# Optimization experiments

Measured on AMD Instinct MI355X. Metric: run time of the kernel, lower is better.

Reference implementation:

```python
import jax, jax.numpy as jnp
import numpy as np

GRID_SIDES = (16, 32, 64)  # levels=3, base_grid_size=16, expansion=2.0, grid_dimensions=2
BATCH, INPUT_DIM = 8192, 256


def setup_inputs() -> dict:
    key = jax.random.key(0)
    k0, k1, k2, k3 = jax.random.split(key, 4)
    x = jax.random.normal(k0, (BATCH, INPUT_DIM), dtype=jnp.float32)
    w1 = jax.random.normal(k1, (GRID_SIDES[0] ** 2, INPUT_DIM), dtype=jnp.float32)
    w2 = jax.random.normal(k2, (GRID_SIDES[1] ** 2, INPUT_DIM), dtype=jnp.float32)
    w3 = jax.random.normal(k3, (GRID_SIDES[2] ** 2, INPUT_DIM), dtype=jnp.float32)
    return {"x": x, "w1": w1, "w2": w2, "w3": w3}


def _som_level(x, w, side):
    # Squared Euclidean distances (B, N) via the expanded form; N = side*side.
    d2 = (
        jnp.sum(x * x, axis=1, keepdims=True)
        - 2.0 * (x @ w.T)
        + jnp.sum(w * w, axis=1)
    )
    bmu_flat = jnp.argmin(d2, axis=1)  # (B,)
    coords = jnp.stack(jnp.unravel_index(bmu_flat, (side, side)), axis=-1)  # (B, 2)
    # Quantization error = exact Euclidean distance to the BMU prototype.
    diff = x - w[bmu_flat]  # (B, D)
    q_err = jnp.sqrt(jnp.sum(diff * diff, axis=1))  # (B,)
    return coords, q_err


def reference(x, w1, w2, w3):
    c1, q1 = _som_level(x, w1, GRID_SIDES[0])
    c2, q2 = _som_level(x, w2, GRID_SIDES[1])
    c3, q3 = _som_level(x, w3, GRID_SIDES[2])
    return (c1, c2, c3, q1, q2, q3)
```

## Files before the change

kernel.cpp:

```cpp
#include <hip/hip_runtime.h>
#include <hip/hip_fp16.h>
#include <stdint.h>

#define DIM 256
#define KE  768
#define NW  5376

typedef _Float16 half8 __attribute__((ext_vector_type(8)));
typedef float floatx4 __attribute__((ext_vector_type(4)));

#define WS_WE_OFF    12582912
#define WS_WNORM_OFF 20840448
#define WS_XNORM_OFF 20861952
#define WS_BEST_OFF  20894720

__global__ __launch_bounds__(256) void conv_kernel(
    const float* __restrict__ x, const float* __restrict__ w1,
    const float* __restrict__ w2, const float* __restrict__ w3,
    ushort* __restrict__ Xe, ushort* __restrict__ We,
    float* __restrict__ wnorm, float* __restrict__ xnorm) {
  int task = blockIdx.x * 4 + (threadIdx.x >> 6);
  int lane = threadIdx.x & 63;
  const float* src; ushort* dst; float* ndst; int isx;
  if (task < 8192) {
    src = x + (size_t)task * DIM; dst = Xe + (size_t)task * KE;
    ndst = xnorm + task; isx = 1;
  } else {
    int wi = task - 8192;
    if (wi < 256)       src = w1 + (size_t)wi * DIM;
    else if (wi < 1280) src = w2 + (size_t)(wi - 256) * DIM;
    else                src = w3 + (size_t)(wi - 1280) * DIM;
    dst = We + (size_t)wi * KE; ndst = wnorm + wi; isx = 0;
  }
  float4 v = *(const float4*)(src + lane * 4);
  float fv[4] = {v.x, v.y, v.z, v.w};
  float s = fv[0]*fv[0] + fv[1]*fv[1] + fv[2]*fv[2] + fv[3]*fv[3];
  #pragma unroll
  for (int o = 32; o > 0; o >>= 1) s += __shfl_xor(s, o);
  if (lane == 0) *ndst = s;

  ushort h[4], l[4];
  #pragma unroll
  for (int e = 0; e < 4; ++e) {
    __half hh = __float2half(fv[e]);
    float hf = __half2float(hh);
    __half ll = __float2half((fv[e] - hf) * 2048.0f);
    h[e] = __half_as_ushort(hh);
    l[e] = __half_as_ushort(ll);
  }
  ushort4 h4 = make_ushort4(h[0], h[1], h[2], h[3]);
  ushort4 l4 = make_ushort4(l[0], l[1], l[2], l[3]);
  if (isx) {
    *(ushort4*)(dst + lane * 4)        = h4;
    *(ushort4*)(dst + 256 + lane * 4)  = h4;
    *(ushort4*)(dst + 512 + lane * 4)  = l4;
  } else {
    *(ushort4*)(dst + lane * 4)        = h4;
    *(ushort4*)(dst + 256 + lane * 4)  = l4;
    *(ushort4*)(dst + 512 + lane * 4)  = h4;
  }
}

__global__ __launch_bounds__(256) void gemm_kernel(
    const ushort* __restrict__ Xe, const ushort* __restrict__ We,
    const float* __restrict__ xnorm, const float* __restrict__ wnorm,
    unsigned long long* __restrict__ best) {
  __shared__ __align__(16) ushort As[128 * 64];
  __shared__ __align__(16) ushort Bs[128 * 64];
  __shared__ unsigned long long red[2][128];

  const int cb = blockIdx.x;
  const int r0 = blockIdx.y * 128;
  const int n0 = cb * 128;
  int level, lbase;
  if (cb < 2)       { level = 0; lbase = 0; }
  else if (cb < 10) { level = 1; lbase = 256; }
  else              { level = 2; lbase = 1280; }

  const int t = threadIdx.x;
  const int w = t >> 6;
  const int lane = t & 63;
  const int ln = lane & 15, q = lane >> 4;
  const int wm = (w >> 1) * 64, wn = (w & 1) * 64;

  floatx4 acc[4][4];
  #pragma unroll
  for (int i = 0; i < 4; ++i)
    #pragma unroll
    for (int j = 0; j < 4; ++j) acc[i][j] = (floatx4)0.0f;

  for (int k0 = 0; k0 < KE; k0 += 64) {
    if (k0 == 256) {
      #pragma unroll
      for (int i = 0; i < 4; ++i)
        #pragma unroll
        for (int j = 0; j < 4; ++j) acc[i][j] *= 2048.0f;
    }
    #pragma unroll
    for (int it = 0; it < 4; ++it) {
      int p = it * 256 + t;
      int m = p >> 3;
      int c = (p & 7) ^ (m & 7);
      const ushort* ga = Xe + (size_t)(r0 + m) * KE + k0 + c * 8;
      const ushort* gb = We + (size_t)(n0 + m) * KE + k0 + c * 8;
      int lbase_chunks = it * 256 + (t & 192);
      __builtin_amdgcn_global_load_lds(
          (const __attribute__((address_space(1))) void*)ga,
          (__attribute__((address_space(3))) void*)(As + lbase_chunks * 8), 16, 0, 0);
      __builtin_amdgcn_global_load_lds(
          (const __attribute__((address_space(1))) void*)gb,
          (__attribute__((address_space(3))) void*)(Bs + lbase_chunks * 8), 16, 0, 0);
    }
    __syncthreads();
    #pragma unroll
    for (int s = 0; s < 2; ++s) {
      half8 a[4], b[4];
      #pragma unroll
      for (int mt = 0; mt < 4; ++mt) {
        int m = wm + mt * 16 + ln;
        int pos = m * 8 + ((s * 4 + q) ^ (m & 7));
        a[mt] = *(const half8*)&As[pos * 8];
      }
      #pragma unroll
      for (int nt = 0; nt < 4; ++nt) {
        int n = wn + nt * 16 + ln;
        int pos = n * 8 + ((s * 4 + q) ^ (n & 7));
        b[nt] = *(const half8*)&Bs[pos * 8];
      }
      #pragma unroll
      for (int mt = 0; mt < 4; ++mt)
        #pragma unroll
        for (int nt = 0; nt < 4; ++nt)
          acc[mt][nt] = __builtin_amdgcn_mfma_f32_16x16x32_f16(
              a[mt], b[nt], acc[mt][nt], 0, 0, 0);
    }
    __syncthreads();
  }

  float wnv[4];
  #pragma unroll
  for (int nt = 0; nt < 4; ++nt) wnv[nt] = wnorm[n0 + wn + nt * 16 + ln];

  #pragma unroll
  for (int mt = 0; mt < 4; ++mt) {
    #pragma unroll
    for (int r = 0; r < 4; ++r) {
      int rowl = wm + mt * 16 + q * 4 + r;
      float xnv = xnorm[r0 + rowl];
      unsigned long long bp = ~0ull;
      #pragma unroll
      for (int nt = 0; nt < 4; ++nt) {
        float d2 = fmaxf(xnv + wnv[nt] - acc[mt][nt][r] * 0.0009765625f, 0.0f);
        unsigned col = (unsigned)(n0 + wn + nt * 16 + ln - lbase);
        unsigned long long p =
            ((unsigned long long)__float_as_uint(d2) << 32) | col;
        bp = (p < bp) ? p : bp;
      }
      #pragma unroll
      for (int off = 1; off < 16; off <<= 1) {
        unsigned long long o = __shfl_xor(bp, off);
        bp = (o < bp) ? o : bp;
      }
      if (ln == 0) red[w & 1][rowl] = bp;
    }
  }
  __syncthreads();
  if (t < 128) {
    unsigned long long a = red[0][t], b = red[1][t];
    unsigned long long m = (a < b) ? a : b;
    atomicMin(&best[level * 8192 + r0 + t], m);
  }
}

__global__ __launch_bounds__(256) void finalize_kernel(
    const float* __restrict__ x, const float* __restrict__ w1,
    const float* __restrict__ w2, const float* __restrict__ w3,
    const unsigned long long* __restrict__ best, float* __restrict__ out) {
  int task = blockIdx.x * 4 + (threadIdx.x >> 6);
  int lane = threadIdx.x & 63;
  int level = task >> 13;
  int row = task & 8191;
  const float* w; unsigned side;
  if (level == 0)      { w = w1; side = 16; }
  else if (level == 1) { w = w2; side = 32; }
  else                 { w = w3; side = 64; }
  unsigned idx = (unsigned)(best[level * 8192 + row] & 0xFFFFFFFFull);
  float4 xv = *(const float4*)(x + (size_t)row * DIM + lane * 4);
  float4 wv = *(const float4*)(w + (size_t)idx * DIM + lane * 4);
  float dx = xv.x - wv.x, dy = xv.y - wv.y, dz = xv.z - wv.z, dw = xv.w - wv.w;
  float s = dx * dx + dy * dy + dz * dz + dw * dw;
  #pragma unroll
  for (int o = 32; o > 0; o >>= 1) s += __shfl_xor(s, o);
  if (lane == 0) {
    out[level * 16384 + row * 2 + 0] = (float)(idx / side);
    out[level * 16384 + row * 2 + 1] = (float)(idx % side);
    out[49152 + level * 8192 + row] = sqrtf(s);
  }
}

extern "C" void kernel_launch(void* const* d_in, const int* in_sizes, int n_in,
                              void* d_out, int out_size, void* d_ws, size_t ws_size,
                              hipStream_t stream) {
  const float* x  = (const float*)d_in[0];
  const float* w1 = (const float*)d_in[1];
  const float* w2 = (const float*)d_in[2];
  const float* w3 = (const float*)d_in[3];
  ushort* Xe = (ushort*)d_ws;
  ushort* We = (ushort*)((char*)d_ws + WS_WE_OFF);
  float* wnorm = (float*)((char*)d_ws + WS_WNORM_OFF);
  float* xnorm = (float*)((char*)d_ws + WS_XNORM_OFF);
  unsigned long long* best = (unsigned long long*)((char*)d_ws + WS_BEST_OFF);

  hipMemsetAsync(best, 0xFF, 24576 * sizeof(unsigned long long), stream);
  conv_kernel<<<3392, 256, 0, stream>>>(x, w1, w2, w3, Xe, We, wnorm, xnorm);
  gemm_kernel<<<dim3(42, 64), 256, 0, stream>>>(Xe, We, xnorm, wnorm, best);
  finalize_kernel<<<6144, 256, 0, stream>>>(x, w1, w2, w3, best, (float*)d_out);
}
```

Baseline: 175.0 us.

## Rewrite split-fp16 GEMM as 256x256 tile with multi-stage LDS pipeline

The distance GEMM now uses 512-thread blocks, each computing a 256x256 output tile. Operands are streamed through a four-slot LDS ring in 32-wide K chunks, with async global-to-LDS loads issued two chunks ahead, phase barriers and MFMA priority raising. The conversion kernel pre-scales the leading hi*hi segment (x by 64, w by 32) so the accumulator no longer needs the mid-loop multiply by 2048. The aim is more reuse per block and load latency hidden behind MFMA work, at the cost of larger LDS and register footprints and fragile hand-written wait counts.

```diff
diff --git a/kernel.cpp b/kernel.cpp
--- a/kernel.cpp
+++ b/kernel.cpp
@@ -39,119 +39,168 @@
   for (int o = 32; o > 0; o >>= 1) s += __shfl_xor(s, o);
   if (lane == 0) *ndst = s;
 
-  ushort h[4], l[4];
+  float scale = isx ? 64.0f : 32.0f;
+  ushort h[4], hs[4], l[4];
   #pragma unroll
   for (int e = 0; e < 4; ++e) {
     __half hh = __float2half(fv[e]);
     float hf = __half2float(hh);
-    __half ll = __float2half((fv[e] - hf) * 2048.0f);
-    h[e] = __half_as_ushort(hh);
-    l[e] = __half_as_ushort(ll);
+    h[e]  = __half_as_ushort(hh);
+    hs[e] = __half_as_ushort(__float2half(hf * scale));
+    l[e]  = __half_as_ushort(__float2half((fv[e] - hf) * 2048.0f));
   }
   ushort4 h4 = make_ushort4(h[0], h[1], h[2], h[3]);
+  ushort4 s4 = make_ushort4(hs[0], hs[1], hs[2], hs[3]);
   ushort4 l4 = make_ushort4(l[0], l[1], l[2], l[3]);
   if (isx) {
-    *(ushort4*)(dst + lane * 4)        = h4;
+    *(ushort4*)(dst + lane * 4)        = s4;
     *(ushort4*)(dst + 256 + lane * 4)  = h4;
     *(ushort4*)(dst + 512 + lane * 4)  = l4;
   } else {
-    *(ushort4*)(dst + lane * 4)        = h4;
+    *(ushort4*)(dst + lane * 4)        = s4;
     *(ushort4*)(dst + 256 + lane * 4)  = l4;
     *(ushort4*)(dst + 512 + lane * 4)  = h4;
   }
 }
 
-__global__ __launch_bounds__(256) void gemm_kernel(
+__global__ __launch_bounds__(512, 2) void gemm_kernel(
     const ushort* __restrict__ Xe, const ushort* __restrict__ We,
     const float* __restrict__ xnorm, const float* __restrict__ wnorm,
     unsigned long long* __restrict__ best) {
-  __shared__ __align__(16) ushort As[128 * 64];
-  __shared__ __align__(16) ushort Bs[128 * 64];
-  __shared__ unsigned long long red[2][128];
-
-  const int cb = blockIdx.x;
-  const int r0 = blockIdx.y * 128;
-  const int n0 = cb * 128;
-  int level, lbase;
-  if (cb < 2)       { level = 0; lbase = 0; }
-  else if (cb < 10) { level = 1; lbase = 256; }
-  else              { level = 2; lbase = 1280; }
+  __shared__ __align__(16) ushort AB[65536];
+  __shared__ unsigned long long red[4][256];
 
   const int t = threadIdx.x;
   const int w = t >> 6;
   const int lane = t & 63;
   const int ln = lane & 15, q = lane >> 4;
-  const int wm = (w >> 1) * 64, wn = (w & 1) * 64;
-
-  floatx4 acc[4][4];
-  #pragma unroll
-  for (int i = 0; i < 4; ++i)
+  const int wr = w >> 2, wc = w & 3;
+  const int r0 = blockIdx.x * 256;
+  const int cb = blockIdx.y;
+  const int n0 = cb << 8;
+  int level, lbase;
+  if (cb < 1)      { level = 0; lbase = 0; }
+  else if (cb < 5) { level = 1; lbase = 256; }
+  else             { level = 2; lbase = 1280; }
+
+  int aoff[2][4], boff[4];
+  #pragma unroll
+  for (int mh = 0; mh < 2; ++mh)
+    #pragma unroll
+    for (int mt = 0; mt < 4; ++mt) {
+      int ra = wr * 128 + mh * 64 + mt * 16 + ln;
+      aoff[mh][mt] = ra * 64 + ((q ^ ((ra >> 1) & 3)) << 4);
+    }
+  #pragma unroll
+  for (int nt = 0; nt < 4; ++nt) {
+    int rb = wc * 64 + nt * 16 + ln;
+    boff[nt] = 65536 + rb * 64 + ((q ^ ((rb >> 1) & 3)) << 4);
+  }
+  const char* ABb = (const char*)AB;
+
+  const int sr = (w << 4) + (lane >> 2);
+  const int sc = lane & 3;
+  const int sg = sc ^ ((sr >> 1) & 3);
+  const ushort* srcA0 = Xe + (size_t)(r0 + sr) * KE + sg * 8;
+  const ushort* srcB0 = We + (size_t)(n0 + sr) * KE + sg * 8;
+  const int ldsO0 = w << 9;
+  const int ldsO1 = 4096 + (w << 9);
+
+#define STAGE_A(hs_) do { const int sl_ = ((hs_) & 3) << 13; \
+    __builtin_amdgcn_global_load_lds( \
+        (const __attribute__((address_space(1))) void*)(srcA0 + (hs_) * 32), \
+        (__attribute__((address_space(3))) void*)(AB + sl_ + ldsO0), 16, 0, 0); \
+    __builtin_amdgcn_global_load_lds( \
+        (const __attribute__((address_space(1))) void*)(srcA0 + 128 * KE + (hs_) * 32), \
+        (__attribute__((address_space(3))) void*)(AB + sl_ + ldsO1), 16, 0, 0); \
+  } while (0)
+#define STAGE_B(hs_) do { const int sl_ = 32768 + (((hs_) & 3) << 13); \
+    __builtin_amdgcn_global_load_lds( \
+        (const __attribute__((address_space(1))) void*)(srcB0 + (hs_) * 32), \
+        (__attribute__((address_space(3))) void*)(AB + sl_ + ldsO0), 16, 0, 0); \
+    __builtin_amdgcn_global_load_lds( \
+        (const __attribute__((address_space(1))) void*)(srcB0 + 128 * KE + (hs_) * 32), \
+        (__attribute__((address_space(3))) void*)(AB + sl_ + ldsO1), 16, 0, 0); \
+  } while (0)
+
+  floatx4 acc[8][4];
+  #pragma unroll
+  for (int i = 0; i < 8; ++i)
     #pragma unroll
     for (int j = 0; j < 4; ++j) acc[i][j] = (floatx4)0.0f;
 
-  for (int k0 = 0; k0 < KE; k0 += 64) {
-    if (k0 == 256) {
-      #pragma unroll
-      for (int i = 0; i < 4; ++i)
-        #pragma unroll
-        for (int j = 0; j < 4; ++j) acc[i][j] *= 2048.0f;
-    }
-    #pragma unroll
-    for (int it = 0; it < 4; ++it) {
-      int p = it * 256 + t;
-      int m = p >> 3;
-      int c = (p & 7) ^ (m & 7);
-      const ushort* ga = Xe + (size_t)(r0 + m) * KE + k0 + c * 8;
-      const ushort* gb = We + (size_t)(n0 + m) * KE + k0 + c * 8;
-      int lbase_chunks = it * 256 + (t & 192);
-      __builtin_amdgcn_global_load_lds(
-          (const __attribute__((address_space(1))) void*)ga,
-          (__attribute__((address_space(3))) void*)(As + lbase_chunks * 8), 16, 0, 0);
-      __builtin_amdgcn_global_load_lds(
-          (const __attribute__((address_space(1))) void*)gb,
-          (__attribute__((address_space(3))) void*)(Bs + lbase_chunks * 8), 16, 0, 0);
-    }
-    __syncthreads();
-    #pragma unroll
-    for (int s = 0; s < 2; ++s) {
-      half8 a[4], b[4];
-      #pragma unroll
-      for (int mt = 0; mt < 4; ++mt) {
-        int m = wm + mt * 16 + ln;
-        int pos = m * 8 + ((s * 4 + q) ^ (m & 7));
-        a[mt] = *(const half8*)&As[pos * 8];
-      }
-      #pragma unroll
-      for (int nt = 0; nt < 4; ++nt) {
-        int n = wn + nt * 16 + ln;
-        int pos = n * 8 + ((s * 4 + q) ^ (n & 7));
-        b[nt] = *(const half8*)&Bs[pos * 8];
-      }
-      #pragma unroll
-      for (int mt = 0; mt < 4; ++mt)
-        #pragma unroll
-        for (int nt = 0; nt < 4; ++nt)
-          acc[mt][nt] = __builtin_amdgcn_mfma_f32_16x16x32_f16(
-              a[mt], b[nt], acc[mt][nt], 0, 0, 0);
-    }
-    __syncthreads();
-  }
+  half8 av[4], bv[4];
+
+  STAGE_A(0); STAGE_B(0); STAGE_A(1); STAGE_B(1);
+  asm volatile("s_waitcnt vmcnt(4)" ::: "memory");
+  __builtin_amdgcn_s_barrier();
+  __builtin_amdgcn_sched_barrier(0);
+
+#define PH0(h_, STG_) { \
+    const int sb_ = ((h_) & 3) << 14; \
+    _Pragma("unroll") for (int mt = 0; mt < 4; ++mt) \
+      av[mt] = *(const half8*)(ABb + sb_ + aoff[0][mt]); \
+    _Pragma("unroll") for (int nt = 0; nt < 4; ++nt) \
+      bv[nt] = *(const half8*)(ABb + sb_ + boff[nt]); \
+    if (STG_) STAGE_A((h_) + 2); \
+    __builtin_amdgcn_sched_barrier(0); \
+    __builtin_amdgcn_s_barrier(); \
+    __builtin_amdgcn_sched_barrier(0); \
+    __builtin_amdgcn_s_setprio(1); \
+    _Pragma("unroll") for (int mt = 0; mt < 4; ++mt) \
+      _Pragma("unroll") for (int nt = 0; nt < 4; ++nt) \
+        acc[mt][nt] = __builtin_amdgcn_mfma_f32_16x16x32_f16( \
+            av[mt], bv[nt], acc[mt][nt], 0, 0, 0); \
+    __builtin_amdgcn_s_setprio(0); \
+    __builtin_amdgcn_sched_barrier(0); \
+    __builtin_amdgcn_s_barrier(); \
+    __builtin_amdgcn_sched_barrier(0); \
+  }
+#define PH1(h_, STG_, VMS_) { \
+    const int sb_ = ((h_) & 3) << 14; \
+    _Pragma("unroll") for (int mt = 0; mt < 4; ++mt) \
+      av[mt] = *(const half8*)(ABb + sb_ + aoff[1][mt]); \
+    if (STG_) STAGE_B((h_) + 2); \
+    __builtin_amdgcn_sched_barrier(0); \
+    __builtin_amdgcn_s_barrier(); \
+    __builtin_amdgcn_sched_barrier(0); \
+    __builtin_amdgcn_s_setprio(1); \
+    _Pragma("unroll") for (int mt = 0; mt < 4; ++mt) \
+      _Pragma("unroll") for (int nt = 0; nt < 4; ++nt) \
+        acc[4 + mt][nt] = __builtin_amdgcn_mfma_f32_16x16x32_f16( \
+            av[mt], bv[nt], acc[4 + mt][nt], 0, 0, 0); \
+    __builtin_amdgcn_s_setprio(0); \
+    VMS_; \
+    __builtin_amdgcn_sched_barrier(0); \
+    __builtin_amdgcn_s_barrier(); \
+    __builtin_amdgcn_sched_barrier(0); \
+  }
+
+  #pragma unroll 1
+  for (int h = 0; h < 22; ++h) {
+    PH0(h, 1);
+    PH1(h, 1, asm volatile("s_waitcnt vmcnt(4)" ::: "memory"));
+  }
+  PH0(22, 0);
+  PH1(22, 0, asm volatile("s_waitcnt vmcnt(0)" ::: "memory"));
+  PH0(23, 0);
+  PH1(23, 0, );
 
   float wnv[4];
   #pragma unroll
-  for (int nt = 0; nt < 4; ++nt) wnv[nt] = wnorm[n0 + wn + nt * 16 + ln];
-
-  #pragma unroll
-  for (int mt = 0; mt < 4; ++mt) {
+  for (int nt = 0; nt < 4; ++nt) wnv[nt] = wnorm[n0 + wc * 64 + nt * 16 + ln];
+
+  #pragma unroll
+  for (int mtg = 0; mtg < 8; ++mtg) {
     #pragma unroll
     for (int r = 0; r < 4; ++r) {
-      int rowl = wm + mt * 16 + q * 4 + r;
+      int rowl = wr * 128 + mtg * 16 + q * 4 + r;
       float xnv = xnorm[r0 + rowl];
       unsigned long long bp = ~0ull;
       #pragma unroll
       for (int nt = 0; nt < 4; ++nt) {
-        float d2 = fmaxf(xnv + wnv[nt] - acc[mt][nt][r] * 0.0009765625f, 0.0f);
-        unsigned col = (unsigned)(n0 + wn + nt * 16 + ln - lbase);
+        float d2 = fmaxf(xnv + wnv[nt] - acc[mtg][nt][r] * 0.0009765625f, 0.0f);
+        unsigned col = (unsigned)(n0 + wc * 64 + nt * 16 + ln - lbase);
         unsigned long long p =
             ((unsigned long long)__float_as_uint(d2) << 32) | col;
         bp = (p < bp) ? p : bp;
@@ -161,13 +210,16 @@
         unsigned long long o = __shfl_xor(bp, off);
         bp = (o < bp) ? o : bp;
       }
-      if (ln == 0) red[w & 1][rowl] = bp;
+      if (ln == 0) red[wc][rowl] = bp;
     }
   }
   __syncthreads();
-  if (t < 128) {
-    unsigned long long a = red[0][t], b = red[1][t];
-    unsigned long long m = (a < b) ? a : b;
+  if (t < 256) {
+    unsigned long long m0 = red[0][t], m1 = red[1][t];
+    unsigned long long m2 = red[2][t], m3 = red[3][t];
+    unsigned long long m = m0 < m1 ? m0 : m1;
+    if (m2 < m) m = m2;
+    if (m3 < m) m = m3;
     atomicMin(&best[level * 8192 + r0 + t], m);
   }
 }
@@ -213,6 +265,6 @@
 
   hipMemsetAsync(best, 0xFF, 24576 * sizeof(unsigned long long), stream);
   conv_kernel<<<3392, 256, 0, stream>>>(x, w1, w2, w3, Xe, We, wnorm, xnorm);
-  gemm_kernel<<<dim3(42, 64), 256, 0, stream>>>(Xe, We, xnorm, wnorm, best);
+  gemm_kernel<<<dim3(32, 21), 512, 0, stream>>>(Xe, We, xnorm, wnorm, best);
   finalize_kernel<<<6144, 256, 0, stream>>>(x, w1, w2, w3, best, (float*)d_out);
 }
```

Result: no change. 174.7 us (-0.2%).

## Add single-pass fp16 screening GEMM with top-2 margin and precise rerun for ambiguous rows

Applied to the files above, without the earlier changes.

The first GEMM now does only a single fp16 pass over K=256 (scaled hi x times hi w) and tracks the best two distances per row. A list-generation kernel marks rows whose top-2 gap is below an error bound derived from the norms. A second GEMM recomputes those rows with the full three-term split precision. This targets the 3x K cost of the split-fp16 GEMM for most rows. In exchange it adds extra kernels, atomics and gathers, and correctness depends on the heuristic threshold constant bounding the fp16 error.

```diff
diff --git a/kernel.cpp b/kernel.cpp
--- a/kernel.cpp
+++ b/kernel.cpp
@@ -4,7 +4,6 @@
 
 #define DIM 256
 #define KE  768
-#define NW  5376
 
 typedef _Float16 half8 __attribute__((ext_vector_type(8)));
 typedef float floatx4 __attribute__((ext_vector_type(4)));
@@ -12,24 +11,28 @@
 #define WS_WE_OFF    12582912
 #define WS_WNORM_OFF 20840448
 #define WS_XNORM_OFF 20861952
-#define WS_BEST_OFF  20894720
+#define WS_M1_OFF    20894720
+#define WS_M2_OFF    21091328
+#define WS_LISTS_OFF 21189632
+#define WS_CTRL_OFF  21287936
 
 __global__ __launch_bounds__(256) void conv_kernel(
     const float* __restrict__ x, const float* __restrict__ w1,
     const float* __restrict__ w2, const float* __restrict__ w3,
     ushort* __restrict__ Xe, ushort* __restrict__ We,
-    float* __restrict__ wnorm, float* __restrict__ xnorm) {
+    float* __restrict__ wnorm, float* __restrict__ xnorm,
+    unsigned* __restrict__ wmaxp) {
   int task = blockIdx.x * 4 + (threadIdx.x >> 6);
   int lane = threadIdx.x & 63;
-  const float* src; ushort* dst; float* ndst; int isx;
+  const float* src; ushort* dst; float* ndst; int isx; int lvl = 0;
   if (task < 8192) {
     src = x + (size_t)task * DIM; dst = Xe + (size_t)task * KE;
     ndst = xnorm + task; isx = 1;
   } else {
     int wi = task - 8192;
-    if (wi < 256)       src = w1 + (size_t)wi * DIM;
-    else if (wi < 1280) src = w2 + (size_t)(wi - 256) * DIM;
-    else                src = w3 + (size_t)(wi - 1280) * DIM;
+    if (wi < 256)       { src = w1 + (size_t)wi * DIM; lvl = 0; }
+    else if (wi < 1280) { src = w2 + (size_t)(wi - 256) * DIM; lvl = 1; }
+    else                { src = w3 + (size_t)(wi - 1280) * DIM; lvl = 2; }
     dst = We + (size_t)wi * KE; ndst = wnorm + wi; isx = 0;
   }
   float4 v = *(const float4*)(src + lane * 4);
@@ -37,37 +40,53 @@
   float s = fv[0]*fv[0] + fv[1]*fv[1] + fv[2]*fv[2] + fv[3]*fv[3];
   #pragma unroll
   for (int o = 32; o > 0; o >>= 1) s += __shfl_xor(s, o);
-  if (lane == 0) *ndst = s;
-
-  ushort h[4], l[4];
+  if (lane == 0) {
+    *ndst = s;
+    if (!isx) atomicMax(wmaxp + lvl, __float_as_uint(s));
+  }
+
+  float scale = isx ? 64.0f : 32.0f;
+  ushort h[4], hs[4], l[4];
   #pragma unroll
   for (int e = 0; e < 4; ++e) {
     __half hh = __float2half(fv[e]);
     float hf = __half2float(hh);
-    __half ll = __float2half((fv[e] - hf) * 2048.0f);
-    h[e] = __half_as_ushort(hh);
-    l[e] = __half_as_ushort(ll);
+    h[e]  = __half_as_ushort(hh);
+    hs[e] = __half_as_ushort(__float2half(hf * scale));
+    l[e]  = __half_as_ushort(__float2half((fv[e] - hf) * 2048.0f));
   }
   ushort4 h4 = make_ushort4(h[0], h[1], h[2], h[3]);
+  ushort4 s4 = make_ushort4(hs[0], hs[1], hs[2], hs[3]);
   ushort4 l4 = make_ushort4(l[0], l[1], l[2], l[3]);
   if (isx) {
-    *(ushort4*)(dst + lane * 4)        = h4;
+    *(ushort4*)(dst + lane * 4)        = s4;
     *(ushort4*)(dst + 256 + lane * 4)  = h4;
     *(ushort4*)(dst + 512 + lane * 4)  = l4;
   } else {
-    *(ushort4*)(dst + lane * 4)        = h4;
+    *(ushort4*)(dst + lane * 4)        = s4;
     *(ushort4*)(dst + 256 + lane * 4)  = l4;
     *(ushort4*)(dst + 512 + lane * 4)  = h4;
   }
 }
 
-__global__ __launch_bounds__(256) void gemm_kernel(
+__device__ __forceinline__ void min2merge(unsigned long long& p1,
+                                          unsigned long long& p2,
+                                          unsigned long long o1,
+                                          unsigned long long o2) {
+  unsigned long long lo = p1 < o1 ? p1 : o1;
+  unsigned long long hi = p1 < o1 ? o1 : p1;
+  unsigned long long mm = p2 < o2 ? p2 : o2;
+  p1 = lo;
+  p2 = hi < mm ? hi : mm;
+}
+
+__global__ __launch_bounds__(256) void gemm1_kernel(
     const ushort* __restrict__ Xe, const ushort* __restrict__ We,
     const float* __restrict__ xnorm, const float* __restrict__ wnorm,
-    unsigned long long* __restrict__ best) {
+    unsigned long long* __restrict__ m1, unsigned* __restrict__ m2) {
   __shared__ __align__(16) ushort As[128 * 64];
   __shared__ __align__(16) ushort Bs[128 * 64];
-  __shared__ unsigned long long red[2][128];
+  __shared__ unsigned long long red1[2][128], red2[2][128];
 
   const int cb = blockIdx.x;
   const int r0 = blockIdx.y * 128;
@@ -89,27 +108,21 @@
     #pragma unroll
     for (int j = 0; j < 4; ++j) acc[i][j] = (floatx4)0.0f;
 
-  for (int k0 = 0; k0 < KE; k0 += 64) {
-    if (k0 == 256) {
-      #pragma unroll
-      for (int i = 0; i < 4; ++i)
-        #pragma unroll
-        for (int j = 0; j < 4; ++j) acc[i][j] *= 2048.0f;
-    }
+  for (int k0 = 0; k0 < 256; k0 += 64) {
     #pragma unroll
     for (int it = 0; it < 4; ++it) {
       int p = it * 256 + t;
       int m = p >> 3;
       int c = (p & 7) ^ (m & 7);
-      const ushort* ga = Xe + (size_t)(r0 + m) * KE + k0 + c * 8;
-      const ushort* gb = We + (size_t)(n0 + m) * KE + k0 + c * 8;
-      int lbase_chunks = it * 256 + (t & 192);
+      const ushort* ga = Xe + (size_t)(r0 + m) * KE + 256 + k0 + c * 8;
+      const ushort* gb = We + (size_t)(n0 + m) * KE + 512 + k0 + c * 8;
+      int lbc = it * 256 + (t & 192);
       __builtin_amdgcn_global_load_lds(
           (const __attribute__((address_space(1))) void*)ga,
-          (__attribute__((address_space(3))) void*)(As + lbase_chunks * 8), 16, 0, 0);
+          (__attribute__((address_space(3))) void*)(As + lbc * 8), 16, 0, 0);
       __builtin_amdgcn_global_load_lds(
           (const __attribute__((address_space(1))) void*)gb,
-          (__attribute__((address_space(3))) void*)(Bs + lbase_chunks * 8), 16, 0, 0);
+          (__attribute__((address_space(3))) void*)(Bs + lbc * 8), 16, 0, 0);
     }
     __syncthreads();
     #pragma unroll
@@ -147,6 +160,148 @@
     for (int r = 0; r < 4; ++r) {
       int rowl = wm + mt * 16 + q * 4 + r;
       float xnv = xnorm[r0 + rowl];
+      unsigned long long p1 = ~0ull, p2 = ~0ull;
+      #pragma unroll
+      for (int nt = 0; nt < 4; ++nt) {
+        float d2 = fmaxf(xnv + wnv[nt] - 2.0f * acc[mt][nt][r], 0.0f);
+        unsigned col = (unsigned)(n0 + wn + nt * 16 + ln - lbase);
+        unsigned long long p =
+            ((unsigned long long)__float_as_uint(d2) << 32) | col;
+        if (p < p1) { p2 = p1; p1 = p; }
+        else if (p < p2) { p2 = p; }
+      }
+      #pragma unroll
+      for (int off = 1; off < 16; off <<= 1) {
+        unsigned long long o1 = __shfl_xor(p1, off);
+        unsigned long long o2 = __shfl_xor(p2, off);
+        min2merge(p1, p2, o1, o2);
+      }
+      if (ln == 0) { red1[w & 1][rowl] = p1; red2[w & 1][rowl] = p2; }
+    }
+  }
+  __syncthreads();
+  if (t < 128) {
+    unsigned long long a1 = red1[0][t], a2 = red2[0][t];
+    min2merge(a1, a2, red1[1][t], red2[1][t]);
+    int slot = level * 8192 + r0 + t;
+    unsigned long long old = atomicMin(&m1[slot], a1);
+    unsigned push = (a1 < old) ? (unsigned)(old >> 32) : (unsigned)(a1 >> 32);
+    atomicMin(&m2[slot], push);
+    atomicMin(&m2[slot], (unsigned)(a2 >> 32));
+  }
+}
+
+__global__ __launch_bounds__(256) void listgen_kernel(
+    unsigned long long* __restrict__ m1, const unsigned* __restrict__ m2,
+    const float* __restrict__ xnorm, const unsigned* __restrict__ ctrl,
+    unsigned* __restrict__ counts, unsigned* __restrict__ lists) {
+  int task = blockIdx.x * 256 + threadIdx.x;
+  if (task >= 24576) return;
+  int level = task >> 13;
+  int row = task & 8191;
+  float d1 = __uint_as_float((unsigned)(m1[task] >> 32));
+  float d2 = __uint_as_float(m2[task]);
+  float th = 0.0045f * sqrtf(xnorm[row] * __uint_as_float(ctrl[level]))
+           + 0.5f;
+  if (!(d2 - d1 > th)) {
+    m1[task] = ~0ull;
+    unsigned pos = atomicAdd(counts + level, 1u);
+    if (pos < 8192u) lists[level * 8192 + pos] = row;
+  }
+}
+
+__global__ __launch_bounds__(256) void gemm2_kernel(
+    const ushort* __restrict__ Xe, const ushort* __restrict__ We,
+    const float* __restrict__ xnorm, const float* __restrict__ wnorm,
+    const unsigned* __restrict__ lists, const unsigned* __restrict__ counts,
+    unsigned long long* __restrict__ m1) {
+  const int cb = blockIdx.x;
+  int level, lbase;
+  if (cb < 2)       { level = 0; lbase = 0; }
+  else if (cb < 10) { level = 1; lbase = 256; }
+  else              { level = 2; lbase = 1280; }
+  const unsigned cnt = counts[level];
+  const unsigned r0i = blockIdx.y * 128;
+  if (r0i >= cnt) return;
+  const unsigned* list = lists + level * 8192;
+
+  __shared__ __align__(16) ushort As[128 * 64];
+  __shared__ __align__(16) ushort Bs[128 * 64];
+  __shared__ unsigned long long red[2][128];
+
+  const int n0 = cb * 128;
+  const int t = threadIdx.x;
+  const int w = t >> 6;
+  const int lane = t & 63;
+  const int ln = lane & 15, q = lane >> 4;
+  const int wm = (w >> 1) * 64, wn = (w & 1) * 64;
+
+  unsigned ar[4];
+  #pragma unroll
+  for (int it = 0; it < 4; ++it) {
+    unsigned li = r0i + it * 32 + (t >> 3);
+    ar[it] = list[li < cnt ? li : (cnt - 1)] & 8191u;
+  }
+
+  floatx4 acc[4][4];
+  #pragma unroll
+  for (int i = 0; i < 4; ++i)
+    #pragma unroll
+    for (int j = 0; j < 4; ++j) acc[i][j] = (floatx4)0.0f;
+
+  for (int k0 = 0; k0 < KE; k0 += 64) {
+    #pragma unroll
+    for (int it = 0; it < 4; ++it) {
+      int p = it * 256 + t;
+      int m = p >> 3;
+      int c = (p & 7) ^ (m & 7);
+      const ushort* ga = Xe + (size_t)ar[it] * KE + k0 + c * 8;
+      const ushort* gb = We + (size_t)(n0 + m) * KE + k0 + c * 8;
+      int lbc = it * 256 + (t & 192);
+      __builtin_amdgcn_global_load_lds(
+          (const __attribute__((address_space(1))) void*)ga,
+          (__attribute__((address_space(3))) void*)(As + lbc * 8), 16, 0, 0);
+      __builtin_amdgcn_global_load_lds(
+          (const __attribute__((address_space(1))) void*)gb,
+          (__attribute__((address_space(3))) void*)(Bs + lbc * 8), 16, 0, 0);
+    }
+    __syncthreads();
+    #pragma unroll
+    for (int s = 0; s < 2; ++s) {
+      half8 a[4], b[4];
+      #pragma unroll
+      for (int mt = 0; mt < 4; ++mt) {
+        int m = wm + mt * 16 + ln;
+        int pos = m * 8 + ((s * 4 + q) ^ (m & 7));
+        a[mt] = *(const half8*)&As[pos * 8];
+      }
+      #pragma unroll
+      for (int nt = 0; nt < 4; ++nt) {
+        int n = wn + nt * 16 + ln;
+        int pos = n * 8 + ((s * 4 + q) ^ (n & 7));
+        b[nt] = *(const half8*)&Bs[pos * 8];
+      }
+      #pragma unroll
+      for (int mt = 0; mt < 4; ++mt)
+        #pragma unroll
+        for (int nt = 0; nt < 4; ++nt)
+          acc[mt][nt] = __builtin_amdgcn_mfma_f32_16x16x32_f16(
+              a[mt], b[nt], acc[mt][nt], 0, 0, 0);
+    }
+    __syncthreads();
+  }
+
+  float wnv[4];
+  #pragma unroll
+  for (int nt = 0; nt < 4; ++nt) wnv[nt] = wnorm[n0 + wn + nt * 16 + ln];
+
+  #pragma unroll
+  for (int mt = 0; mt < 4; ++mt) {
+    #pragma unroll
+    for (int r = 0; r < 4; ++r) {
+      int rowl = wm + mt * 16 + q * 4 + r;
+      unsigned li = r0i + rowl;
+      float xnv = xnorm[list[li < cnt ? li : (cnt - 1)] & 8191u];
       unsigned long long bp = ~0ull;
       #pragma unroll
       for (int nt = 0; nt < 4; ++nt) {
@@ -165,17 +320,17 @@
     }
   }
   __syncthreads();
-  if (t < 128) {
+  if (t < 128 && r0i + t < cnt) {
     unsigned long long a = red[0][t], b = red[1][t];
     unsigned long long m = (a < b) ? a : b;
-    atomicMin(&best[level * 8192 + r0 + t], m);
+    atomicMin(&m1[level * 8192 + (list[r0i + t] & 8191u)], m);
   }
 }
 
 __global__ __launch_bounds__(256) void finalize_kernel(
     const float* __restrict__ x, const float* __restrict__ w1,
     const float* __restrict__ w2, const float* __restrict__ w3,
-    const unsigned long long* __restrict__ best, float* __restrict__ out) {
+    const unsigned long long* __restrict__ m1, float* __restrict__ out) {
   int task = blockIdx.x * 4 + (threadIdx.x >> 6);
   int lane = threadIdx.x & 63;
   int level = task >> 13;
@@ -184,7 +339,8 @@
   if (level == 0)      { w = w1; side = 16; }
   else if (level == 1) { w = w2; side = 32; }
   else                 { w = w3; side = 64; }
-  unsigned idx = (unsigned)(best[level * 8192 + row] & 0xFFFFFFFFull);
+  unsigned idx = (unsigned)(m1[task] & 0xFFFFFFFFull);
+  if (idx >= side * side) idx = 0;
   float4 xv = *(const float4*)(x + (size_t)row * DIM + lane * 4);
   float4 wv = *(const float4*)(w + (size_t)idx * DIM + lane * 4);
   float dx = xv.x - wv.x, dy = xv.y - wv.y, dz = xv.z - wv.z, dw = xv.w - wv.w;
@@ -209,10 +365,19 @@
   ushort* We = (ushort*)((char*)d_ws + WS_WE_OFF);
   float* wnorm = (float*)((char*)d_ws + WS_WNORM_OFF);
   float* xnorm = (float*)((char*)d_ws + WS_XNORM_OFF);
-  unsigned long long* best = (unsigned long long*)((char*)d_ws + WS_BEST_OFF);
-
-  hipMemsetAsync(best, 0xFF, 24576 * sizeof(unsigned long long), stream);
-  conv_kernel<<<3392, 256, 0, stream>>>(x, w1, w2, w3, Xe, We, wnorm, xnorm);
-  gemm_kernel<<<dim3(42, 64), 256, 0, stream>>>(Xe, We, xnorm, wnorm, best);
-  finalize_kernel<<<6144, 256, 0, stream>>>(x, w1, w2, w3, best, (float*)d_out);
-}
+  unsigned long long* m1 = (unsigned long long*)((char*)d_ws + WS_M1_OFF);
+  unsigned* m2 = (unsigned*)((char*)d_ws + WS_M2_OFF);
+  unsigned* lists = (unsigned*)((char*)d_ws + WS_LISTS_OFF);
+  unsigned* ctrl  = (unsigned*)((char*)d_ws + WS_CTRL_OFF);
+  unsigned* counts = ctrl + 4;
+
+  hipMemsetAsync(m1, 0xFF, 24576 * 8 + 24576 * 4, stream);
+  hipMemsetAsync(ctrl, 0, 64, stream);
+  conv_kernel<<<3392, 256, 0, stream>>>(x, w1, w2, w3, Xe, We, wnorm, xnorm,
+                                        ctrl);
+  gemm1_kernel<<<dim3(42, 64), 256, 0, stream>>>(Xe, We, xnorm, wnorm, m1, m2);
+  listgen_kernel<<<96, 256, 0, stream>>>(m1, m2, xnorm, ctrl, counts, lists);
+  gemm2_kernel<<<dim3(42, 64), 256, 0, stream>>>(Xe, We, xnorm, wnorm, lists,
+                                                 counts, m1);
+  finalize_kernel<<<6144, 256, 0, stream>>>(x, w1, w2, w3, m1, (float*)d_out);
+}
```

Measured after the change: 293.5 us. 67.6% more time.
